# Optimization experiments

Hardware: AMD Instinct MI355X
Metric: run time of the kernel (lower is better)

## Reference

```python
import math
import jax, jax.numpy as jnp
import numpy as np

HIDDEN = 1024
HEADS = 16
HEAD = HIDDEN // HEADS
BUCKET = 32
MAXPOS = 512
REL = 2 * BUCKET - 1
EPS = 1e-7
L, B = 512, 16
STD = math.sqrt(2.0 / (5.0 * HIDDEN))


def _ln(x, g=None, b=None):
    m = x.mean(-1, keepdims=True)
    v = ((x - m) ** 2).mean(-1, keepdims=True)
    y = (x - m) * jax.lax.rsqrt(v + EPS)
    return y if g is None else y * g + b


def _bucket_indices(n):
    # DeBERTa-style log bucket relative positions, shifted to [0, 2*BUCKET-2]
    r = jnp.arange(n)[:, None] - jnp.arange(n)[None, :]
    mid = BUCKET // 2
    abs_pos = jnp.where((r < mid) & (r > -mid), mid - 1,
                        jnp.clip(jnp.abs(r), None, MAXPOS - 1))
    log_pos = jnp.ceil(jnp.log(abs_pos.astype(jnp.float32) / mid)
                       / math.log((MAXPOS - 1) / mid) * (mid - 1)).astype(jnp.int32) + mid
    bucket_pos = jnp.where(abs_pos <= mid, r, log_pos * jnp.sign(r))
    return (BUCKET - 1 + bucket_pos).astype(jnp.int32)


def setup_inputs() -> dict:
    key = jax.random.key(0)
    ks = jax.random.split(key, 8)
    return {
        'hidden_states': jax.random.normal(ks[0], (L, B, HIDDEN), jnp.float32),
        'attention_mask': jax.random.randint(ks[1], (B, 1, 1, L), 0, 2).astype(bool),
        'relative_embedding': jax.random.normal(ks[2], (REL, HIDDEN), jnp.float32),
        'wqk': jax.random.normal(ks[3], (2 * HIDDEN, HIDDEN), jnp.float32) * STD,
        'bqk': jnp.zeros((2 * HIDDEN,), jnp.float32),
        'wv': jax.random.normal(ks[4], (HIDDEN, HIDDEN), jnp.float32) * STD,
        'bv': jnp.zeros((HIDDEN,), jnp.float32),
        'wo': jax.random.normal(ks[5], (HIDDEN, HIDDEN), jnp.float32) * STD,
        'bo': jnp.zeros((HIDDEN,), jnp.float32),
        'ln_g': jnp.ones((HIDDEN,), jnp.float32),
        'ln_b': jnp.zeros((HIDDEN,), jnp.float32),
    }


def reference(hidden_states, attention_mask, relative_embedding,
              wqk, bqk, wv, bv, wo, bo, ln_g, ln_b):
    Lq, Bq, D = hidden_states.shape
    scale = 1.0 / math.sqrt(3 * HEAD)
    h = _ln(hidden_states)                                 # pre LN, no affine
    q, k = jnp.split(h @ wqk.T + bqk, 2, axis=-1)
    v = h @ wv.T + bv
    qpos, kpos = jnp.split(relative_embedding @ wqk.T + bqk, 2, axis=-1)
    qpos = qpos.reshape(REL, HEADS, HEAD)
    kpos = kpos.reshape(REL, HEADS, HEAD)
    # (L,B,D) -> (B,H,L,hd)
    qh = q.reshape(Lq, Bq, HEADS, HEAD).transpose(1, 2, 0, 3)
    kh = k.reshape(Lq, Bq, HEADS, HEAD).transpose(1, 2, 0, 3)
    vh = v.reshape(Lq, Bq, HEADS, HEAD).transpose(1, 2, 0, 3)
    scores = jnp.einsum('bhqd,bhkd->bhqk', qh, kh) * scale       # c2c
    qp = jnp.einsum('bhqd,khd->bhqk', qh, kpos) * scale          # c2p (k over buckets)
    pk = jnp.einsum('bhkd,qhd->bhqk', kh, qpos) * scale          # p2c (q over buckets)
    idx = jnp.broadcast_to(_bucket_indices(Lq), (Bq, HEADS, Lq, Lq))
    scores = scores + jnp.take_along_axis(qp, idx, axis=-1) \
                    + jnp.take_along_axis(pk, idx, axis=-2)
    # masked softmax: mask==True -> -inf before softmax, 0 after
    probs = jax.nn.softmax(jnp.where(attention_mask, -1e9, scores), axis=-1)
    probs = jnp.where(attention_mask, 0.0, probs)
    ctx = jnp.einsum('bhqk,bhkd->bhqd', probs, vh)
    ctx = ctx.transpose(2, 0, 1, 3).reshape(Lq, Bq, D)           # (L,B,D)
    out = ctx @ wo.T + bo
    return _ln(out, ln_g, ln_b)
```

## Files before the change

kernel.cpp:

```cpp
#include <hip/hip_runtime.h>
#include <hip/hip_bf16.h>

#define HID 1024
#define HEADS 16
#define HEAD 64
#define RELN 63
#define SEQ 512
#define BATCH 16
#define NROWS (SEQ*BATCH)
#define MEXT 8320
#define NQKV 3072
#define LNEPS 1e-7f
#define SCALE2 (0.07216878364870323f * 1.4426950408889634f)

typedef __attribute__((ext_vector_type(4))) float  f32x4;
typedef __attribute__((ext_vector_type(8))) short  s16x8;
typedef __attribute__((ext_vector_type(4))) ushort u16x4;

static __device__ __forceinline__ ushort f2bf(float f) {
  union { float f; unsigned u; } v; v.f = f;
  unsigned r = v.u + 0x7fffu + ((v.u >> 16) & 1u);
  return (ushort)(r >> 16);
}
static __device__ __forceinline__ float bf2f(ushort u) {
  union { unsigned u; float f; } v; v.u = ((unsigned)u) << 16;
  return v.f;
}

__global__ void k_prep(const void* mask_raw, const float* bqk, const float* bv,
                       ushort* mask01, int* idx_tab, float* bcat) {
  __shared__ int s_isbool;
  int tid = threadIdx.x;
  if (tid == 0) s_isbool = 0;
  __syncthreads();
  const unsigned* mu = (const unsigned*)mask_raw;
  int bad = 0;
  for (int i = tid; i < 2048; i += 256) if (mu[i] > 1u) bad = 1;
  if (bad) s_isbool = 1;
  __syncthreads();
  int isbool = s_isbool;
  const unsigned char* m8 = (const unsigned char*)mask_raw;
  const int* m32 = (const int*)mask_raw;
  for (int i = tid; i < BATCH*SEQ; i += 256) {
    int m = isbool ? (int)m8[i] : m32[i];
    mask01[i] = m ? 1 : 0;
  }
  for (int i = tid; i < 1023; i += 256) {
    int r = i - 511;
    int a = r < 0 ? -r : r;
    int absp = (a < 16) ? 15 : (a < 511 ? a : 511);
    int idx;
    if (absp <= 16) idx = 31 + r;
    else {
      float v = logf((float)absp / 16.0f) / logf(511.0f / 16.0f) * 15.0f;
      int lp = (int)ceilf(v) + 16;
      idx = 31 + (r > 0 ? lp : -lp);
    }
    idx_tab[i] = idx;
  }
  for (int i = tid; i < 2048; i += 256) bcat[i] = bqk[i];
  for (int i = tid; i < 1024; i += 256) bcat[2048 + i] = bv[i];
}

__global__ void k_convert(const float* wqk, const float* wv, const float* wo,
                          ushort* wcat, ushort* wo_b) {
  int i = blockIdx.x * 256 + threadIdx.x;
  if (i < 2048 * 1024) wcat[i] = f2bf(wqk[i]);
  else if (i < 3072 * 1024) wcat[i] = f2bf(wv[i - 2048 * 1024]);
  if (i < 1024 * 1024) wo_b[i] = f2bf(wo[i]);
}

__global__ __launch_bounds__(256) void k_ln1(const float* hid, const float* rel, ushort* h_ext) {
  int row = blockIdx.x, tid = threadIdx.x;
  __shared__ float red[8];
  if (row < NROWS) {
    const float* src = hid + (size_t)row * HID;
    f32x4 x = *(const f32x4*)(src + tid * 4);
    float s = x[0] + x[1] + x[2] + x[3];
    #pragma unroll
    for (int m = 1; m < 64; m <<= 1) s += __shfl_xor(s, m);
    if ((tid & 63) == 0) red[tid >> 6] = s;
    __syncthreads();
    float mean = (red[0] + red[1] + red[2] + red[3]) * (1.0f / HID);
    float d0 = x[0] - mean, d1 = x[1] - mean, d2 = x[2] - mean, d3 = x[3] - mean;
    float sq = d0*d0 + d1*d1 + d2*d2 + d3*d3;
    #pragma unroll
    for (int m = 1; m < 64; m <<= 1) sq += __shfl_xor(sq, m);
    __syncthreads();
    if ((tid & 63) == 0) red[4 + (tid >> 6)] = sq;
    __syncthreads();
    float var = (red[4] + red[5] + red[6] + red[7]) * (1.0f / HID);
    float rs = rsqrtf(var + LNEPS);
    u16x4 o = { f2bf(d0*rs), f2bf(d1*rs), f2bf(d2*rs), f2bf(d3*rs) };
    *(u16x4*)(h_ext + (size_t)row * HID + tid * 4) = o;
  } else if (row < NROWS + RELN) {
    const float* src = rel + (size_t)(row - NROWS) * HID;
    f32x4 x = *(const f32x4*)(src + tid * 4);
    u16x4 o = { f2bf(x[0]), f2bf(x[1]), f2bf(x[2]), f2bf(x[3]) };
    *(u16x4*)(h_ext + (size_t)row * HID + tid * 4) = o;
  } else {
    u16x4 z = { 0, 0, 0, 0 };
    *(u16x4*)(h_ext + (size_t)row * HID + tid * 4) = z;
  }
}

template<int WRITE_F32>
__global__ __launch_bounds__(256) void k_gemm(const ushort* A, const ushort* Bw, const float* bias,
                                              ushort* Cb, float* Cf, int M, int N, int K) {
  __shared__ char smem[32768];
  char* As = smem;
  char* Bs = smem + 16384;
  int tid = threadIdx.x, lane = tid & 63, w = tid >> 6;
  int nbn = N >> 7;
  int per = gridDim.x >> 3;
  int gl = (blockIdx.x & 7) * per + (blockIdx.x >> 3);
  int bm = gl / nbn, bn = gl % nbn;
  int wr = w >> 1, wc = w & 1;
  int g = lane >> 4, r = lane & 15;
  f32x4 acc[4][4] = {};
  for (int ko = 0; ko < K; ko += 64) {
    __syncthreads();
    #pragma unroll
    for (int c = 0; c < 4; ++c) {
      int chunk = c * 256 + tid;
      int row = chunk >> 3;
      int kb = (chunk & 7) << 4;
      int kbs = kb ^ ((row & 7) << 4);
      const char* gA = (const char*)(A + (size_t)(bm * 128 + row) * K + ko) + kbs;
      const char* gB = (const char*)(Bw + (size_t)(bn * 128 + row) * K + ko) + kbs;
      __builtin_amdgcn_global_load_lds((const __attribute__((address_space(1))) void*)gA,
                                       (__attribute__((address_space(3))) void*)(As + c * 4096 + w * 1024),
                                       16, 0, 0);
      __builtin_amdgcn_global_load_lds((const __attribute__((address_space(1))) void*)gB,
                                       (__attribute__((address_space(3))) void*)(Bs + c * 4096 + w * 1024),
                                       16, 0, 0);
    }
    __syncthreads();
    #pragma unroll
    for (int kk = 0; kk < 2; ++kk) {
      s16x8 af[4], bf[4];
      #pragma unroll
      for (int mt = 0; mt < 4; ++mt) {
        int row = wr * 64 + mt * 16 + r;
        int kb = (kk * 64 + g * 16) ^ ((row & 7) << 4);
        af[mt] = *(const s16x8*)(As + row * 128 + kb);
      }
      #pragma unroll
      for (int nt = 0; nt < 4; ++nt) {
        int row = wc * 64 + nt * 16 + r;
        int kb = (kk * 64 + g * 16) ^ ((row & 7) << 4);
        bf[nt] = *(const s16x8*)(Bs + row * 128 + kb);
      }
      #pragma unroll
      for (int mt = 0; mt < 4; ++mt)
        #pragma unroll
        for (int nt = 0; nt < 4; ++nt)
          acc[mt][nt] = __builtin_amdgcn_mfma_f32_16x16x32_bf16(af[mt], bf[nt], acc[mt][nt], 0, 0, 0);
    }
  }
  #pragma unroll
  for (int nt = 0; nt < 4; ++nt) {
    int col = bn * 128 + wc * 64 + nt * 16 + r;
    float bvv = bias[col];
    #pragma unroll
    for (int mt = 0; mt < 4; ++mt) {
      int row0 = bm * 128 + wr * 64 + mt * 16 + g * 4;
      #pragma unroll
      for (int i = 0; i < 4; ++i) {
        float v = acc[mt][nt][i] + bvv;
        if (WRITE_F32) Cf[(size_t)(row0 + i) * N + col] = v;
        else           Cb[(size_t)(row0 + i) * N + col] = f2bf(v);
      }
    }
  }
}

__global__ __launch_bounds__(256) void k_pos(const ushort* qkv, const ushort* mask01,
                                             ushort* qp, ushort* pk) {
  int bh = blockIdx.x;
  int b = bh >> 4, h = bh & 15;
  int tid = threadIdx.x, lane = tid & 63, w = tid >> 6;
  int g = lane >> 4, r = lane & 15;
  __shared__ ushort mb[512];
  for (int i = tid; i < 512; i += 256) mb[i] = mask01[b * SEQ + i];
  __syncthreads();
  s16x8 bkp[4][2], bqp[4][2];
  #pragma unroll
  for (int nt = 0; nt < 4; ++nt)
    #pragma unroll
    for (int kk = 0; kk < 2; ++kk) {
      size_t rowp = (size_t)(NROWS + nt * 16 + r);
      int colq = h * 64 + kk * 32 + g * 8;
      bqp[nt][kk] = *(const s16x8*)(qkv + rowp * NQKV + colq);
      bkp[nt][kk] = *(const s16x8*)(qkv + rowp * NQKV + 1024 + colq);
    }
  for (int cc = 0; cc < 8; ++cc) {
    int rowbase = cc * 64 + w * 16;
    s16x8 aq[2], ak[2];
    #pragma unroll
    for (int kk = 0; kk < 2; ++kk) {
      size_t rowq = (size_t)((rowbase + r) * 16 + b);
      int colq = h * 64 + kk * 32 + g * 8;
      aq[kk] = *(const s16x8*)(qkv + rowq * NQKV + colq);
      ak[kk] = *(const s16x8*)(qkv + rowq * NQKV + 1024 + colq);
    }
    f32x4 accq[4] = {}, acck[4] = {};
    #pragma unroll
    for (int kk = 0; kk < 2; ++kk)
      #pragma unroll
      for (int nt = 0; nt < 4; ++nt) {
        accq[nt] = __builtin_amdgcn_mfma_f32_16x16x32_bf16(aq[kk], bkp[nt][kk], accq[nt], 0, 0, 0);
        acck[nt] = __builtin_amdgcn_mfma_f32_16x16x32_bf16(ak[kk], bqp[nt][kk], acck[nt], 0, 0, 0);
      }
    #pragma unroll
    for (int nt = 0; nt < 4; ++nt)
      #pragma unroll
      for (int i = 0; i < 4; ++i) {
        int q = rowbase + g * 4 + i;
        int t = nt * 16 + r;
        float biasv = mb[q] ? -1e9f : 0.0f;
        qp[(size_t)bh * SEQ * 64 + q * 64 + t] = f2bf(accq[nt][i] * SCALE2);
        pk[(size_t)bh * SEQ * 64 + q * 64 + t] = f2bf(acck[nt][i] * SCALE2 + biasv);
      }
  }
}

__global__ __launch_bounds__(256) void k_vt(const ushort* qkv, ushort* vt, ushort* kc) {
  int bid = blockIdx.x;
  int bh = bid >> 3, lt = bid & 7;
  int b = bh >> 4, h = bh & 15;
  __shared__ ushort tile[64][72];
  int tid = threadIdx.x;
  #pragma unroll
  for (int c = 0; c < 2; ++c) {
    int e = (c * 256 + tid) * 8;
    int l = e >> 6, d0 = e & 63;
    size_t row = (size_t)((lt * 64 + l) * 16 + b);
    s16x8 kv = *(const s16x8*)(qkv + row * NQKV + 1024 + h * 64 + d0);
    #pragma unroll
    for (int j = 0; j < 8; ++j) kv[j] = (short)f2bf(bf2f((ushort)kv[j]) * SCALE2);
    *(s16x8*)(kc + ((size_t)bh * SEQ + lt * 64 + l) * 64 + d0) = kv;
    *(s16x8*)&tile[l][d0] = *(const s16x8*)(qkv + row * NQKV + 2048 + h * 64 + d0);
  }
  __syncthreads();
  #pragma unroll
  for (int c = 0; c < 2; ++c) {
    int e = (c * 256 + tid) * 8;
    int d = e >> 6, l0 = e & 63;
    ushort tmp[8];
    #pragma unroll
    for (int j = 0; j < 8; ++j) tmp[j] = tile[l0 + j][d];
    *(s16x8*)(vt + (size_t)(bh * 64 + d) * SEQ + lt * 64 + l0) = *(s16x8*)tmp;
  }
}

__global__ __launch_bounds__(256) void k_attn(const ushort* qkv, const ushort* qp_all, const ushort* pk_all,
                                              const ushort* kc, const ushort* vt,
                                              const int* idx_tab, ushort* ctx) {
  int bid = blockIdx.x;
  int slot = bid >> 3;
  int bh = (bid & 7) * 32 + (slot >> 3);
  int qt = slot & 7;
  int b = bh >> 4, h = bh & 15;
  int tid = threadIdx.x, lane = tid & 63, w = tid >> 6;
  int g = lane >> 4, r = lane & 15;

  __shared__ char   Ks[8192];
  __shared__ ushort qp_s[64][72];
  __shared__ ushort pk_s[64][72];
  __shared__ ushort p_s[4][16][72];
  __shared__ unsigned char idx_s[1024];

  const size_t qp_base = (size_t)bh * SEQ * 64 + (size_t)qt * 4096;
  const size_t pk_base = (size_t)bh * SEQ * 64;
  const char* kcb = (const char*)(kc + (size_t)bh * SEQ * 64);

  int krow = w * 8 + (lane >> 3);
  int ksrccol = ((lane & 7) ^ (lane >> 3)) << 4;

  #pragma unroll
  for (int c = 0; c < 2; ++c) {
    const char* src = kcb + (size_t)(c * 32 + krow) * 128 + ksrccol;
    __builtin_amdgcn_global_load_lds((const __attribute__((address_space(1))) void*)src,
                                     (__attribute__((address_space(3))) void*)(Ks + c * 4096 + w * 1024),
                                     16, 0, 0);
  }
  s16x8 pkreg[2];
  #pragma unroll
  for (int c = 0; c < 2; ++c)
    pkreg[c] = *(const s16x8*)(pk_all + pk_base + (size_t)(c * 256 + tid) * 8);
  #pragma unroll
  for (int c = 0; c < 2; ++c) {
    int chunk = c * 256 + tid;
    s16x8 v = *(const s16x8*)(qp_all + qp_base + (size_t)chunk * 8);
    *(s16x8*)&qp_s[chunk >> 3][(chunk & 7) * 8] = v;
  }
  for (int i = tid; i < 1023; i += 256) idx_s[i] = (unsigned char)idx_tab[i];
  s16x8 aq[2];
  int qg0 = qt * 64 + w * 16;
  #pragma unroll
  for (int kk = 0; kk < 2; ++kk) {
    size_t row = (size_t)((qg0 + r) * 16 + b);
    aq[kk] = *(const s16x8*)(qkv + row * NQKV + h * 64 + kk * 32 + g * 8);
  }
  #pragma unroll
  for (int c = 0; c < 2; ++c) {
    int chunk = c * 256 + tid;
    *(s16x8*)&pk_s[chunk >> 3][(chunk & 7) * 8] = pkreg[c];
  }
  __syncthreads();

  float m_i = -3e38f, l_i = 0.0f;
  f32x4 o_acc[4] = {};
  const ushort* qprow = &qp_s[w * 16 + r][0];
  const int qglob511 = qt * 64 + w * 16 + r + 511;

  for (int kt = 0; kt < 8; ++kt) {
    if (kt < 7) {
      #pragma unroll
      for (int c = 0; c < 2; ++c)
        pkreg[c] = *(const s16x8*)(pk_all + pk_base + (size_t)(kt + 1) * 4096 + (size_t)(c * 256 + tid) * 8);
    }

    f32x4 s[4];
    #pragma unroll
    for (int nt = 0; nt < 4; ++nt) {
      f32x4 a = {};
      #pragma unroll
      for (int kk = 0; kk < 2; ++kk) {
        s16x8 bk = *(const s16x8*)(Ks + (nt * 16 + r) * 128 + ((kk * 64 + g * 16) ^ ((r & 7) << 4)));
        a = __builtin_amdgcn_mfma_f32_16x16x32_bf16(bk, aq[kk], a, 0, 0, 0);
      }
      s[nt] = a;
    }

    float m_loc = -3e38f;
    #pragma unroll
    for (int nt = 0; nt < 4; ++nt) {
      #pragma unroll
      for (int i = 0; i < 4; ++i) {
        int kl = nt * 16 + g * 4 + i;
        int t = idx_s[qglob511 - kt * 64 - kl];
        float v = s[nt][i] + bf2f(qprow[t]) + bf2f(pk_s[kl][t]);
        s[nt][i] = v;
        m_loc = fmaxf(m_loc, v);
      }
    }
    __syncthreads();

    if (kt < 7) {
      #pragma unroll
      for (int c = 0; c < 2; ++c) {
        const char* src = kcb + (size_t)(kt + 1) * 8192 + (size_t)(c * 32 + krow) * 128 + ksrccol;
        __builtin_amdgcn_global_load_lds((const __attribute__((address_space(1))) void*)src,
                                         (__attribute__((address_space(3))) void*)(Ks + c * 4096 + w * 1024),
                                         16, 0, 0);
      }
      #pragma unroll
      for (int c = 0; c < 2; ++c) {
        int chunk = c * 256 + tid;
        *(s16x8*)&pk_s[chunk >> 3][(chunk & 7) * 8] = pkreg[c];
      }
    }
    s16x8 vreg[2][4];
    #pragma unroll
    for (int kk = 0; kk < 2; ++kk)
      #pragma unroll
      for (int nt = 0; nt < 4; ++nt)
        vreg[kk][nt] = *(const s16x8*)(vt + (size_t)(bh * 64 + nt * 16 + r) * SEQ + kt * 64 + kk * 32 + g * 8);

    float mx = fmaxf(m_loc, __shfl_xor(m_loc, 16));
    mx = fmaxf(mx, __shfl_xor(mx, 32));

    if (__any(mx > m_i + 8.0f)) {
      float mnew = fmaxf(m_i, mx);
      float rs = exp2f(m_i - mnew);
      m_i = mnew;
      l_i *= rs;
      float rsb[4];
      #pragma unroll
      for (int i = 0; i < 4; ++i) rsb[i] = __shfl(rs, g * 4 + i);
      #pragma unroll
      for (int nt = 0; nt < 4; ++nt)
        #pragma unroll
        for (int i = 0; i < 4; ++i) o_acc[nt][i] *= rsb[i];
    }

    float psum = 0.0f;
    #pragma unroll
    for (int nt = 0; nt < 4; ++nt) {
      u16x4 pk4;
      #pragma unroll
      for (int i = 0; i < 4; ++i) {
        float pe = exp2f(s[nt][i] - m_i);
        psum += pe;
        pk4[i] = f2bf(pe);
      }
      *(u16x4*)&p_s[w][r][nt * 16 + g * 4] = pk4;
    }
    psum += __shfl_xor(psum, 16);
    psum += __shfl_xor(psum, 32);
    l_i += psum;

    #pragma unroll
    for (int kk = 0; kk < 2; ++kk) {
      s16x8 pa = *(const s16x8*)&p_s[w][r][kk * 32 + g * 8];
      #pragma unroll
      for (int nt = 0; nt < 4; ++nt)
        o_acc[nt] = __builtin_amdgcn_mfma_f32_16x16x32_bf16(pa, vreg[kk][nt], o_acc[nt], 0, 0, 0);
    }

    if (kt < 7) __syncthreads();
  }

  float lb[4];
  #pragma unroll
  for (int i = 0; i < 4; ++i) lb[i] = __shfl(l_i, g * 4 + i);
  #pragma unroll
  for (int i = 0; i < 4; ++i) {
    float inv = lb[i] > 0.0f ? 1.0f / lb[i] : 0.0f;
    int lq = qt * 64 + w * 16 + g * 4 + i;
    size_t rowc = (size_t)(lq * 16 + b);
    #pragma unroll
    for (int nt = 0; nt < 4; ++nt)
      ctx[rowc * HID + h * 64 + nt * 16 + r] = f2bf(o_acc[nt][i] * inv);
  }
}

__global__ __launch_bounds__(256) void k_ln2(const ushort* tmpb, const float* gamma, const float* beta,
                                             float* out) {
  int row = blockIdx.x, tid = threadIdx.x;
  __shared__ float red[8];
  u16x4 xb = *(const u16x4*)(tmpb + (size_t)row * HID + tid * 4);
  float x[4] = { bf2f(xb[0]), bf2f(xb[1]), bf2f(xb[2]), bf2f(xb[3]) };
  float s = x[0] + x[1] + x[2] + x[3];
  #pragma unroll
  for (int m = 1; m < 64; m <<= 1) s += __shfl_xor(s, m);
  if ((tid & 63) == 0) red[tid >> 6] = s;
  __syncthreads();
  float mean = (red[0] + red[1] + red[2] + red[3]) * (1.0f / HID);
  float d[4]; float sq = 0.0f;
  #pragma unroll
  for (int j = 0; j < 4; ++j) { d[j] = x[j] - mean; sq += d[j] * d[j]; }
  #pragma unroll
  for (int m = 1; m < 64; m <<= 1) sq += __shfl_xor(sq, m);
  __syncthreads();
  if ((tid & 63) == 0) red[4 + (tid >> 6)] = sq;
  __syncthreads();
  float var = (red[4] + red[5] + red[6] + red[7]) * (1.0f / HID);
  float rs = rsqrtf(var + LNEPS);
  f32x4 o;
  #pragma unroll
  for (int j = 0; j < 4; ++j) o[j] = d[j] * rs * gamma[tid * 4 + j] + beta[tid * 4 + j];
  *(f32x4*)(out + (size_t)row * HID + tid * 4) = o;
}

extern "C" void kernel_launch(void* const* d_in, const int* in_sizes, int n_in,
                              void* d_out, int out_size, void* d_ws, size_t ws_size,
                              hipStream_t stream) {
  (void)in_sizes; (void)n_in; (void)out_size; (void)ws_size;
  const float* hid  = (const float*)d_in[0];
  const void*  mask = d_in[1];
  const float* rel  = (const float*)d_in[2];
  const float* wqk  = (const float*)d_in[3];
  const float* bqk  = (const float*)d_in[4];
  const float* wv   = (const float*)d_in[5];
  const float* bv   = (const float*)d_in[6];
  const float* wo   = (const float*)d_in[7];
  const float* bo   = (const float*)d_in[8];
  const float* ln_g = (const float*)d_in[9];
  const float* ln_b = (const float*)d_in[10];

  char* ws = (char*)d_ws;
  ushort* wcat     = (ushort*)(ws);
  ushort* wo_b     = (ushort*)(ws + 6291456);
  float*  bcat     = (float*) (ws + 8388608);
  ushort* mask01   = (ushort*)(ws + 8400896);
  int*    idx_tab  = (int*)   (ws + 8433664);
  ushort* h_ext    = (ushort*)(ws + 8437760);
  ushort* qkv      = (ushort*)(ws + 25477120);
  ushort* qp_b     = (ushort*)(ws + 76595200);
  ushort* pk_b     = (ushort*)(ws + 93372416);
  ushort* vt       = (ushort*)(ws + 110149632);
  char*   tmpr     = (ws + 126926848);
  ushort* ctx = h_ext;
  ushort* kc   = (ushort*)tmpr;
  ushort* tmpb = (ushort*)tmpr;

  k_prep<<<1, 256, 0, stream>>>(mask, bqk, bv, mask01, idx_tab, bcat);
  k_convert<<<12288, 256, 0, stream>>>(wqk, wv, wo, wcat, wo_b);
  k_ln1<<<MEXT, 256, 0, stream>>>(hid, rel, h_ext);
  k_gemm<0><<<(MEXT / 128) * (NQKV / 128), 256, 0, stream>>>(h_ext, wcat, bcat, qkv, nullptr, MEXT, NQKV, 1024);
  k_pos<<<256, 256, 0, stream>>>(qkv, mask01, qp_b, pk_b);
  k_vt<<<2048, 256, 0, stream>>>(qkv, vt, kc);
  k_attn<<<2048, 256, 0, stream>>>(qkv, qp_b, pk_b, kc, vt, idx_tab, ctx);
  k_gemm<0><<<(NROWS / 128) * (1024 / 128), 256, 0, stream>>>(ctx, wo_b, bo, tmpb, nullptr, NROWS, 1024, 1024);
  k_ln2<<<NROWS, 256, 0, stream>>>(tmpb, ln_g, ln_b, (float*)d_out);
}
```

Baseline: 281.0 us.

## Process two query tiles per attention block and vectorize weight conversion

After: 265.3 us. -5.6%, faster.

```diff
diff --git a/kernel.cpp b/kernel.cpp
--- a/kernel.cpp
+++ b/kernel.cpp
@@ -62,12 +62,15 @@
   for (int i = tid; i < 1024; i += 256) bcat[2048 + i] = bv[i];
 }
 
-__global__ void k_convert(const float* wqk, const float* wv, const float* wo,
-                          ushort* wcat, ushort* wo_b) {
-  int i = blockIdx.x * 256 + threadIdx.x;
-  if (i < 2048 * 1024) wcat[i] = f2bf(wqk[i]);
-  else if (i < 3072 * 1024) wcat[i] = f2bf(wv[i - 2048 * 1024]);
-  if (i < 1024 * 1024) wo_b[i] = f2bf(wo[i]);
+__global__ __launch_bounds__(256) void k_convert(const float* wqk, const float* wv, const float* wo,
+                                                 ushort* wcat, ushort* wo_b) {
+  int c = blockIdx.x * 256 + threadIdx.x;
+  f32x4 x; ushort* dst;
+  if (c < 524288)      { x = *(const f32x4*)(wqk + (size_t)c * 4);            dst = wcat + (size_t)c * 4; }
+  else if (c < 786432) { x = *(const f32x4*)(wv  + (size_t)(c - 524288) * 4); dst = wcat + (size_t)c * 4; }
+  else                 { x = *(const f32x4*)(wo  + (size_t)(c - 786432) * 4); dst = wo_b + (size_t)(c - 786432) * 4; }
+  u16x4 o = { f2bf(x[0]), f2bf(x[1]), f2bf(x[2]), f2bf(x[3]) };
+  *(u16x4*)dst = o;
 }
 
 __global__ __launch_bounds__(256) void k_ln1(const float* hid, const float* rel, ushort* h_ext) {
@@ -254,73 +257,69 @@
   }
 }
 
-__global__ __launch_bounds__(256) void k_attn(const ushort* qkv, const ushort* qp_all, const ushort* pk_all,
+__global__ __launch_bounds__(512) void k_attn(const ushort* qkv, const ushort* qp_all, const ushort* pk_all,
                                               const ushort* kc, const ushort* vt,
                                               const int* idx_tab, ushort* ctx) {
   int bid = blockIdx.x;
   int slot = bid >> 3;
-  int bh = (bid & 7) * 32 + (slot >> 3);
-  int qt = slot & 7;
+  int bh = (bid & 7) * 32 + (slot >> 2);
+  int qt0 = (slot & 3) * 2;
   int b = bh >> 4, h = bh & 15;
   int tid = threadIdx.x, lane = tid & 63, w = tid >> 6;
   int g = lane >> 4, r = lane & 15;
+  int qsub = w >> 2, wq = w & 3;
 
   __shared__ char   Ks[8192];
-  __shared__ ushort qp_s[64][72];
-  __shared__ ushort pk_s[64][72];
-  __shared__ ushort p_s[4][16][72];
-  __shared__ unsigned char idx_s[1024];
-
-  const size_t qp_base = (size_t)bh * SEQ * 64 + (size_t)qt * 4096;
+  __shared__ ushort qp_s[128][68];
+  __shared__ ushort pk_s[64][68];
+  __shared__ ushort p_s[8][16][68];
+  __shared__ ushort idx_s[1024];
+
+  const size_t qp_base = (size_t)bh * SEQ * 64 + (size_t)qt0 * 4096;
   const size_t pk_base = (size_t)bh * SEQ * 64;
   const char* kcb = (const char*)(kc + (size_t)bh * SEQ * 64);
 
-  int krow = w * 8 + (lane >> 3);
-  int ksrccol = ((lane & 7) ^ (lane >> 3)) << 4;
-
-  #pragma unroll
-  for (int c = 0; c < 2; ++c) {
-    const char* src = kcb + (size_t)(c * 32 + krow) * 128 + ksrccol;
+  int krow = tid >> 3;
+  int ksrccol = ((tid & 7) ^ (krow & 7)) << 4;
+  int prow = tid >> 3, pcol8 = (tid & 7) * 8;
+
+  {
+    const char* src = kcb + (size_t)krow * 128 + ksrccol;
     __builtin_amdgcn_global_load_lds((const __attribute__((address_space(1))) void*)src,
-                                     (__attribute__((address_space(3))) void*)(Ks + c * 4096 + w * 1024),
+                                     (__attribute__((address_space(3))) void*)(Ks + w * 1024),
                                      16, 0, 0);
   }
-  s16x8 pkreg[2];
-  #pragma unroll
-  for (int c = 0; c < 2; ++c)
-    pkreg[c] = *(const s16x8*)(pk_all + pk_base + (size_t)(c * 256 + tid) * 8);
-  #pragma unroll
-  for (int c = 0; c < 2; ++c) {
-    int chunk = c * 256 + tid;
-    s16x8 v = *(const s16x8*)(qp_all + qp_base + (size_t)chunk * 8);
-    *(s16x8*)&qp_s[chunk >> 3][(chunk & 7) * 8] = v;
-  }
-  for (int i = tid; i < 1023; i += 256) idx_s[i] = (unsigned char)idx_tab[i];
+  s16x8 pkreg = *(const s16x8*)(pk_all + pk_base + (size_t)tid * 8);
+  #pragma unroll
+  for (int c = 0; c < 4; ++c) {
+    int chunk = c * 512 + tid;
+    int row = chunk >> 4, col4 = (chunk & 15) * 4;
+    *(u16x4*)&qp_s[row][col4] = *(const u16x4*)(qp_all + qp_base + (size_t)row * 64 + col4);
+  }
+  for (int i = tid; i < 1023; i += 512) idx_s[i] = (ushort)idx_tab[i];
   s16x8 aq[2];
-  int qg0 = qt * 64 + w * 16;
+  int qg0 = (qt0 + qsub) * 64 + wq * 16;
   #pragma unroll
   for (int kk = 0; kk < 2; ++kk) {
     size_t row = (size_t)((qg0 + r) * 16 + b);
     aq[kk] = *(const s16x8*)(qkv + row * NQKV + h * 64 + kk * 32 + g * 8);
   }
-  #pragma unroll
-  for (int c = 0; c < 2; ++c) {
-    int chunk = c * 256 + tid;
-    *(s16x8*)&pk_s[chunk >> 3][(chunk & 7) * 8] = pkreg[c];
+  {
+    u16x4 lo = { (ushort)pkreg[0], (ushort)pkreg[1], (ushort)pkreg[2], (ushort)pkreg[3] };
+    u16x4 hi = { (ushort)pkreg[4], (ushort)pkreg[5], (ushort)pkreg[6], (ushort)pkreg[7] };
+    *(u16x4*)&pk_s[prow][pcol8] = lo;
+    *(u16x4*)&pk_s[prow][pcol8 + 4] = hi;
   }
   __syncthreads();
 
   float m_i = -3e38f, l_i = 0.0f;
   f32x4 o_acc[4] = {};
-  const ushort* qprow = &qp_s[w * 16 + r][0];
-  const int qglob511 = qt * 64 + w * 16 + r + 511;
+  const ushort* qprow = &qp_s[qsub * 64 + wq * 16 + r][0];
+  const int qglob511 = (qt0 + qsub) * 64 + wq * 16 + r + 511;
 
   for (int kt = 0; kt < 8; ++kt) {
-    if (kt < 7) {
-      #pragma unroll
-      for (int c = 0; c < 2; ++c)
-        pkreg[c] = *(const s16x8*)(pk_all + pk_base + (size_t)(kt + 1) * 4096 + (size_t)(c * 256 + tid) * 8);
-    }
+    if (kt < 7)
+      pkreg = *(const s16x8*)(pk_all + pk_base + (size_t)(kt + 1) * 4096 + (size_t)tid * 8);
 
     f32x4 s[4];
     #pragma unroll
@@ -349,18 +348,14 @@
     __syncthreads();
 
     if (kt < 7) {
-      #pragma unroll
-      for (int c = 0; c < 2; ++c) {
-        const char* src = kcb + (size_t)(kt + 1) * 8192 + (size_t)(c * 32 + krow) * 128 + ksrccol;
-        __builtin_amdgcn_global_load_lds((const __attribute__((address_space(1))) void*)src,
-                                         (__attribute__((address_space(3))) void*)(Ks + c * 4096 + w * 1024),
-                                         16, 0, 0);
-      }
-      #pragma unroll
-      for (int c = 0; c < 2; ++c) {
-        int chunk = c * 256 + tid;
-        *(s16x8*)&pk_s[chunk >> 3][(chunk & 7) * 8] = pkreg[c];
-      }
+      const char* src = kcb + (size_t)(kt + 1) * 8192 + (size_t)krow * 128 + ksrccol;
+      __builtin_amdgcn_global_load_lds((const __attribute__((address_space(1))) void*)src,
+                                       (__attribute__((address_space(3))) void*)(Ks + w * 1024),
+                                       16, 0, 0);
+      u16x4 lo = { (ushort)pkreg[0], (ushort)pkreg[1], (ushort)pkreg[2], (ushort)pkreg[3] };
+      u16x4 hi = { (ushort)pkreg[4], (ushort)pkreg[5], (ushort)pkreg[6], (ushort)pkreg[7] };
+      *(u16x4*)&pk_s[prow][pcol8] = lo;
+      *(u16x4*)&pk_s[prow][pcol8 + 4] = hi;
     }
     s16x8 vreg[2][4];
     #pragma unroll
@@ -404,7 +399,10 @@
 
     #pragma unroll
     for (int kk = 0; kk < 2; ++kk) {
-      s16x8 pa = *(const s16x8*)&p_s[w][r][kk * 32 + g * 8];
+      u16x4 lo = *(const u16x4*)&p_s[w][r][kk * 32 + g * 8];
+      u16x4 hi = *(const u16x4*)&p_s[w][r][kk * 32 + g * 8 + 4];
+      s16x8 pa = { (short)lo[0], (short)lo[1], (short)lo[2], (short)lo[3],
+                   (short)hi[0], (short)hi[1], (short)hi[2], (short)hi[3] };
       #pragma unroll
       for (int nt = 0; nt < 4; ++nt)
         o_acc[nt] = __builtin_amdgcn_mfma_f32_16x16x32_bf16(pa, vreg[kk][nt], o_acc[nt], 0, 0, 0);
@@ -419,7 +417,7 @@
   #pragma unroll
   for (int i = 0; i < 4; ++i) {
     float inv = lb[i] > 0.0f ? 1.0f / lb[i] : 0.0f;
-    int lq = qt * 64 + w * 16 + g * 4 + i;
+    int lq = (qt0 + qsub) * 64 + wq * 16 + g * 4 + i;
     size_t rowc = (size_t)(lq * 16 + b);
     #pragma unroll
     for (int nt = 0; nt < 4; ++nt)
@@ -488,12 +486,12 @@
   ushort* tmpb = (ushort*)tmpr;
 
   k_prep<<<1, 256, 0, stream>>>(mask, bqk, bv, mask01, idx_tab, bcat);
-  k_convert<<<12288, 256, 0, stream>>>(wqk, wv, wo, wcat, wo_b);
+  k_convert<<<4096, 256, 0, stream>>>(wqk, wv, wo, wcat, wo_b);
   k_ln1<<<MEXT, 256, 0, stream>>>(hid, rel, h_ext);
   k_gemm<0><<<(MEXT / 128) * (NQKV / 128), 256, 0, stream>>>(h_ext, wcat, bcat, qkv, nullptr, MEXT, NQKV, 1024);
   k_pos<<<256, 256, 0, stream>>>(qkv, mask01, qp_b, pk_b);
   k_vt<<<2048, 256, 0, stream>>>(qkv, vt, kc);
-  k_attn<<<2048, 256, 0, stream>>>(qkv, qp_b, pk_b, kc, vt, idx_tab, ctx);
+  k_attn<<<1024, 512, 0, stream>>>(qkv, qp_b, pk_b, kc, vt, idx_tab, ctx);
   k_gemm<0><<<(NROWS / 128) * (1024 / 128), 256, 0, stream>>>(ctx, wo_b, bo, tmpb, nullptr, NROWS, 1024, 1024);
   k_ln2<<<NROWS, 256, 0, stream>>>(tmpb, ln_g, ln_b, (float*)d_out);
 }
```
